# Kernel optimization log

Measured on AMD Instinct MI355X. Metric: run time of the kernel, lower is better.

The kernel has to match this reference:

```python
import jax, jax.numpy as jnp
import numpy as np

DIM = 256
HEADS = 8
WS = 8
N = WS * WS
HID = 1024
EPS = 1e-5


def _rel_pos_index():
    ch, cw = np.meshgrid(np.arange(WS), np.arange(WS), indexing='ij')
    coords = np.stack([ch.ravel(), cw.ravel()])  # [2, N]
    rel = coords[:, :, None] - coords[:, None, :]  # [2, N, N]
    rel = rel.transpose(1, 2, 0).astype(np.int64)
    rel[:, :, 0] += WS - 1
    rel[:, :, 1] += WS - 1
    rel[:, :, 0] *= 2 * WS - 1
    return jnp.asarray(rel.sum(-1))  # [N, N]

REL_IDX = _rel_pos_index()


def layer_norm(x, g, b):
    mu = jnp.mean(x, axis=-1, keepdims=True)
    var = jnp.mean(jnp.square(x - mu), axis=-1, keepdims=True)
    return (x - mu) * jax.lax.rsqrt(var + EPS) * g + b


def setup_inputs() -> dict:
    key = jax.random.key(0)
    ks = jax.random.split(key, 12)
    s = 0.02
    return {
        'x': jax.random.normal(ks[0], (32, 4096, DIM), jnp.float32),
        'attn_mask': jnp.zeros((64, N, N), jnp.float32),  # unused (forward sets mask=None)
        'g1': jnp.ones((DIM,), jnp.float32),
        'b1': jnp.zeros((DIM,), jnp.float32),
        'w_qkv': jax.random.normal(ks[1], (3 * DIM, DIM), jnp.float32) * s,
        'b_qkv': jnp.zeros((3 * DIM,), jnp.float32),
        'bias_table': jax.random.normal(ks[2], ((2 * WS - 1) ** 2, HEADS), jnp.float32) * s,
        'w_proj': jax.random.normal(ks[3], (DIM, DIM), jnp.float32) * s,
        'b_proj': jnp.zeros((DIM,), jnp.float32),
        'g2': jnp.ones((DIM,), jnp.float32),
        'b2': jnp.zeros((DIM,), jnp.float32),
        'w_fc1': jax.random.normal(ks[4], (HID, DIM), jnp.float32) * s,
        'b_fc1': jnp.zeros((HID,), jnp.float32),
        'w_fc2': jax.random.normal(ks[5], (DIM, HID), jnp.float32) * s,
        'b_fc2': jnp.zeros((DIM,), jnp.float32),
    }


def reference(x, attn_mask, g1, b1, w_qkv, b_qkv, bias_table, w_proj, b_proj,
              g2, b2, w_fc1, b_fc1, w_fc2, b_fc2):
    B, L, C = x.shape
    H = W = int(np.sqrt(L))
    hd = C // HEADS
    scale = hd ** -0.5

    shortcut = x
    xn = layer_norm(x, g1, b1).reshape(B, H, W, C)
    xw = xn.reshape(B, H // WS, WS, W // WS, WS, C)
    xw = xw.transpose(0, 1, 3, 2, 4, 5).reshape(-1, N, C)  # [B_, N, C]

    qkv = (xw @ w_qkv.T + b_qkv).reshape(-1, N, 3, HEADS, hd)
    q, k, v = [qkv[:, :, i].transpose(0, 2, 1, 3) for i in range(3)]  # [B_, h, N, d]
    attn = jnp.einsum('bhnd,bhmd->bhnm', q * scale, k)
    bias = bias_table[REL_IDX]  # [N, N, h]
    attn = attn + bias.transpose(2, 0, 1)[None]
    attn = jax.nn.softmax(attn, axis=-1)
    out = jnp.einsum('bhnm,bhmd->bhnd', attn, v)
    out = out.transpose(0, 2, 1, 3).reshape(-1, N, C)
    out = out @ w_proj.T + b_proj

    # window reverse
    out = out.reshape(B, H // WS, W // WS, WS, WS, C)
    out = out.transpose(0, 1, 3, 2, 4, 5).reshape(B, L, C)

    x1 = shortcut + out
    h = layer_norm(x1, g2, b2) @ w_fc1.T + b_fc1
    h = jax.nn.gelu(h, approximate=False)
    return x1 + (h @ w_fc2.T + b_fc2)
```

## Files before the change

kernel.cpp:

```cpp
#include <hip/hip_runtime.h>
#include <hip/hip_bf16.h>
#include <hip/hip_fp16.h>

typedef _Float16 f16;
typedef __attribute__((ext_vector_type(8))) _Float16 f16x8;
typedef __attribute__((ext_vector_type(4))) _Float16 f16x4;
typedef __attribute__((ext_vector_type(2))) _Float16 f16x2;
typedef __attribute__((ext_vector_type(4))) float f32x4;

#define AS1(p) ((const __attribute__((address_space(1))) void*)(p))
#define AS3(p) ((__attribute__((address_space(3))) void*)(p))

__global__ __launch_bounds__(256) void cvt_weights(
    const float* __restrict__ wq, const float* __restrict__ wp,
    const float* __restrict__ wf1, const float* __restrict__ wf2,
    f16* __restrict__ o) {
  int i = blockIdx.x * 256 + threadIdx.x;
  float v;
  if (i < 196608)       v = wq[i];
  else if (i < 262144)  v = wp[i - 196608];
  else if (i < 524288)  v = wf1[i - 262144];
  else                  v = wf2[i - 524288];
  o[i] = (f16)v;
}

__global__ __launch_bounds__(256) void prep_bias(
    const float* __restrict__ bt, float* __restrict__ T) {
  const int flat = blockIdx.x * 256 + threadIdx.x;
  const int h = flat >> 12, l = (flat >> 6) & 63, s = flat & 63;
  const int i = s >> 4, j = (s >> 2) & 3, r = s & 3;
  const int n = 16 * i + 4 * (l >> 4) + r;
  const int m = 16 * j + (l & 15);
  const int idx = ((n >> 3) - (m >> 3) + 7) * 15 + ((n & 7) - (m & 7) + 7);
  T[flat] = bt[idx * 8 + h] * 1.4426950408889634f;
}

template<bool PART, typename TIN>
__global__ __launch_bounds__(256) void ln_rows(
    const TIN* __restrict__ x, const float* __restrict__ g,
    const float* __restrict__ b, f16* __restrict__ out) {
  const int t = blockIdx.x * 4 + (threadIdx.x >> 6);
  const int lane = threadIdx.x & 63;
  float v0, v1, v2, v3;
  if constexpr (sizeof(TIN) == 4) {
    const float4 v = ((const float4*)(x + (long)t * 256))[lane];
    v0 = v.x; v1 = v.y; v2 = v.z; v3 = v.w;
  } else {
    const f16x4 v = ((const f16x4*)(x + (long)t * 256))[lane];
    v0 = (float)v[0]; v1 = (float)v[1]; v2 = (float)v[2]; v3 = (float)v[3];
  }
  float s  = v0 + v1 + v2 + v3;
  float ss = v0*v0 + v1*v1 + v2*v2 + v3*v3;
  #pragma unroll
  for (int off = 32; off; off >>= 1) {
    s  += __shfl_xor(s, off);
    ss += __shfl_xor(ss, off);
  }
  const float mu = s * (1.0f / 256.0f);
  const float var = ss * (1.0f / 256.0f) - mu * mu;
  const float rs = rsqrtf(var + 1e-5f);
  const float4 gv = ((const float4*)g)[lane];
  const float4 bv = ((const float4*)b)[lane];
  long row;
  if (PART) {
    const int bI = t >> 12, l = t & 4095;
    const int hh = l >> 6, w2 = l & 63;
    const int wi = bI * 64 + (hh >> 3) * 8 + (w2 >> 3);
    const int n  = (hh & 7) * 8 + (w2 & 7);
    row = (long)wi * 64 + n;
  } else {
    row = t;
  }
  f16x4 o4;
  o4[0] = (f16)((v0 - mu) * rs * gv.x + bv.x);
  o4[1] = (f16)((v1 - mu) * rs * gv.y + bv.y);
  o4[2] = (f16)((v2 - mu) * rs * gv.z + bv.z);
  o4[3] = (f16)((v3 - mu) * rs * gv.w + bv.w);
  *(f16x4*)(out + row * 256 + lane * 4) = o4;
}

template<int EPI, int K>
__global__ __launch_bounds__(256) void gemm_bt(
    const f16* __restrict__ A, const f16* __restrict__ Bw,
    const float* __restrict__ bias, const float* __restrict__ residf,
    const f16* __restrict__ residh,
    f16* __restrict__ outh, float* __restrict__ outf, int N) {
  __shared__ f16 As[2][128 * 64];
  __shared__ f16 Bs[2][128 * 64];
  const int tid  = threadIdx.x;
  const int wid  = tid >> 6;
  const int lane = tid & 63;
  const int qd   = lane >> 4;
  const int l16  = lane & 15;
  const int gx  = gridDim.x;
  const int nwg = gx * gridDim.y;
  const int g   = blockIdx.y * gx + blockIdx.x;
  const int gs  = (g & 7) * (nwg >> 3) + (g >> 3);
  const long tM = (long)(gs / gx) * 128;
  const int  tN = (gs % gx) * 128;
  const int sgrow = lane >> 3;
  const int scol  = ((lane & 7) ^ sgrow) * 8;
  const int wm = (wid >> 1) * 64;
  const int wn = (wid & 1) * 64;

  f32x4 acc[4][4];
  #pragma unroll
  for (int i = 0; i < 4; ++i)
    #pragma unroll
    for (int j = 0; j < 4; ++j) acc[i][j] = (f32x4){0.f, 0.f, 0.f, 0.f};

  const int nt = K / 64;
  f16x8 af[2][4], bf[2][4];

  auto stage_tile = [&](int tt) {
    const int k0 = tt * 64;
    f16* Ad = &As[tt & 1][0];
    f16* Bd = &Bs[tt & 1][0];
    #pragma unroll
    for (int u = 0; u < 4; ++u) {
      const int gidx = wid * 4 + u;
      const int row  = gidx * 8 + sgrow;
      __builtin_amdgcn_global_load_lds(AS1(A + (tM + row) * K + k0 + scol),
                                       AS3(&Ad[gidx * 512]), 16, 0, 0);
      __builtin_amdgcn_global_load_lds(AS1(Bw + (long)(tN + row) * K + k0 + scol),
                                       AS3(&Bd[gidx * 512]), 16, 0, 0);
    }
  };
  auto load_frags = [&](int cb) {
    #pragma unroll
    for (int kk = 0; kk < 2; ++kk) {
      #pragma unroll
      for (int i = 0; i < 4; ++i) {
        const int row = wm + i * 16 + l16;
        af[kk][i] = *(const f16x8*)&As[cb][row * 64 + (((kk << 2) | qd) ^ (row & 7)) * 8];
      }
      #pragma unroll
      for (int j = 0; j < 4; ++j) {
        const int row = wn + j * 16 + l16;
        bf[kk][j] = *(const f16x8*)&Bs[cb][row * 64 + (((kk << 2) | qd) ^ (row & 7)) * 8];
      }
    }
  };
  auto do_mfma = [&]() {
    #pragma unroll
    for (int kk = 0; kk < 2; ++kk)
      #pragma unroll
      for (int i = 0; i < 4; ++i)
        #pragma unroll
        for (int j = 0; j < 4; ++j)
          acc[i][j] = __builtin_amdgcn_mfma_f32_16x16x32_f16(af[kk][i], bf[kk][j], acc[i][j], 0, 0, 0);
  };

  stage_tile(0);
  stage_tile(1);

  for (int t = 0; t < nt - 2; ++t) {
    asm volatile("s_waitcnt vmcnt(8)" ::: "memory");
    __builtin_amdgcn_s_barrier();
    load_frags(t & 1);
    asm volatile("s_waitcnt lgkmcnt(0)" ::: "memory");
    __builtin_amdgcn_s_barrier();
    stage_tile(t + 2);
    do_mfma();
  }
  asm volatile("s_waitcnt vmcnt(8)" ::: "memory");
  __builtin_amdgcn_s_barrier();
  load_frags(nt & 1);
  do_mfma();
  asm volatile("s_waitcnt vmcnt(0)" ::: "memory");
  __builtin_amdgcn_s_barrier();
  load_frags((nt - 1) & 1);
  do_mfma();

  float bb[4];
  #pragma unroll
  for (int j = 0; j < 4; ++j) bb[j] = bias[tN + wn + j * 16 + l16];

  if (EPI == 3) {
    #pragma unroll
    for (int j = 0; j < 4; ++j) {
      const int col = tN + wn + j * 16 + l16;
      #pragma unroll
      for (int i = 0; i < 4; ++i) {
        #pragma unroll
        for (int r = 0; r < 4; ++r) {
          const long row = tM + wm + i * 16 + qd * 4 + r;
          const long off = row * 256 + col;
          outf[off] = (float)residh[off] + acc[i][j][r] + bb[j];
        }
      }
    }
  } else {
    __syncthreads();
    f16* slice = &As[0][0] + wid * 1024;
    const int rrow = lane >> 3;
    const int seg  = lane & 7;
    #pragma unroll
    for (int i = 0; i < 4; ++i) {
      #pragma unroll
      for (int j = 0; j < 4; ++j) {
        #pragma unroll
        for (int r = 0; r < 4; ++r) {
          float v = acc[i][j][r] + bb[j];
          if (EPI == 2) {
            const float u2 = v * v;
            const float w  = v * (-2.3022082f - 0.10294324f * u2);
            const float e  = __builtin_amdgcn_exp2f(w);
            v = v * __builtin_amdgcn_rcpf(1.0f + e);
          }
          const int r16 = qd * 4 + r;
          slice[r16 * 64 + ((j * 16 + l16) ^ ((r16 & 7) << 3))] = (f16)v;
        }
      }
      __syncthreads();
      #pragma unroll
      for (int hrow = 0; hrow < 16; hrow += 8) {
        const int lrow = hrow + rrow;
        const f16x8 v8 = *(const f16x8*)(slice + lrow * 64 + (seg ^ (lrow & 7)) * 8);
        const long grow = tM + wm + i * 16 + lrow;
        const int  gc   = tN + wn + seg * 8;
        if (EPI == 1) {
          const int rw = (int)grow;
          const int wi = rw >> 6, n = rw & 63;
          const int bI = wi >> 6, wloc = wi & 63;
          const int hh = (wloc >> 3) * 8 + (n >> 3);
          const int w2 = (wloc & 7) * 8 + (n & 7);
          const long prow = (long)bI * 4096 + hh * 64 + w2;
          const float* rp = residf + prow * 256 + gc;
          f16x8 o;
          #pragma unroll
          for (int k = 0; k < 8; ++k) o[k] = (f16)(rp[k] + (float)v8[k]);
          *(f16x8*)(outh + prow * 256 + gc) = o;
        } else {
          *(f16x8*)(outh + grow * N + gc) = v8;
        }
      }
      __syncthreads();
    }
  }
}

__global__ __launch_bounds__(256, 3) void attn_win(
    const f16* __restrict__ qkv, const float* __restrict__ bt,
    f16* __restrict__ out) {
  __shared__ __align__(16) char SMEM[4 * 12800];
  const int wid = threadIdx.x >> 6, lane = threadIdx.x & 63;
  const int qd = lane >> 4, l16 = lane & 15;
  const int unit = blockIdx.x * 4 + wid;
  const int wi = unit >> 3, h = unit & 7;
  char* W = SMEM + wid * 12800;
  f16* VT = (f16*)W;
  char* Pb = W + 4608;

  const f16* qbase = qkv + (long)wi * 64 * 768 + h * 32;

  f16x8 qa[4], kb[4];
  #pragma unroll
  for (int i = 0; i < 4; ++i)
    qa[i] = *(const f16x8*)(qbase + (16 * i + l16) * 768 + qd * 8);
  #pragma unroll
  for (int j = 0; j < 4; ++j)
    kb[j] = *(const f16x8*)(qbase + 256 + (16 * j + l16) * 768 + qd * 8);

  #pragma unroll
  for (int it = 0; it < 4; ++it) {
    const f16x8 v8 = *(const f16x8*)(qbase + 512 + (16 * it + l16) * 768 + qd * 8);
    #pragma unroll
    for (int e = 0; e < 8; ++e)
      VT[(qd * 8 + e) * 72 + 16 * it + l16] = v8[e];
  }

  f32x4 S[4][4];
  #pragma unroll
  for (int i = 0; i < 4; ++i)
    #pragma unroll
    for (int j = 0; j < 4; ++j) S[i][j] = (f32x4){0.f, 0.f, 0.f, 0.f};
  #pragma unroll
  for (int i = 0; i < 4; ++i)
    #pragma unroll
    for (int j = 0; j < 4; ++j)
      S[i][j] = __builtin_amdgcn_mfma_f32_16x16x32_f16(qa[i], kb[j], S[i][j], 0, 0, 0);

  const float SC = 0.17677669529663687f * 1.4426950408889634f;
  const float* Tb = bt + ((h * 64 + lane) << 6);
  #pragma unroll
  for (int i = 0; i < 4; ++i) {
    f32x4 b0 = *(const f32x4*)(Tb + i * 16);
    f32x4 b1 = *(const f32x4*)(Tb + i * 16 + 4);
    f32x4 b2 = *(const f32x4*)(Tb + i * 16 + 8);
    f32x4 b3 = *(const f32x4*)(Tb + i * 16 + 12);
    #pragma unroll
    for (int r = 0; r < 4; ++r) {
      S[i][0][r] = S[i][0][r] * SC + b0[r];
      S[i][1][r] = S[i][1][r] * SC + b1[r];
      S[i][2][r] = S[i][2][r] * SC + b2[r];
      S[i][3][r] = S[i][3][r] * SC + b3[r];
    }
  }

  float inv[4][4];
  #pragma unroll
  for (int i = 0; i < 4; ++i) {
    #pragma unroll
    for (int r = 0; r < 4; ++r) {
      float mx = fmaxf(fmaxf(S[i][0][r], S[i][1][r]), fmaxf(S[i][2][r], S[i][3][r]));
      #pragma unroll
      for (int msk = 1; msk < 16; msk <<= 1) mx = fmaxf(mx, __shfl_xor(mx, msk));
      float s0 = 0.f;
      #pragma unroll
      for (int j = 0; j < 4; ++j) {
        const float p = __builtin_amdgcn_exp2f(S[i][j][r] - mx);
        S[i][j][r] = p;
        s0 += p;
      }
      #pragma unroll
      for (int msk = 1; msk < 16; msk <<= 1) s0 += __shfl_xor(s0, msk);
      inv[i][r] = __builtin_amdgcn_rcpf(s0);
    }
  }

  #pragma unroll
  for (int i = 0; i < 4; ++i) {
    #pragma unroll
    for (int r = 0; r < 4; ++r) {
      const int n = 16 * i + 4 * qd + r;
      char* rowp = Pb + n * 128;
      const int sw = (n & 7) << 4;
      #pragma unroll
      for (int j = 0; j < 4; ++j)
        *(f16*)(rowp + ((j * 32 + l16 * 2) ^ sw)) = (f16)S[i][j][r];
    }
  }

  f32x4 O[4][2];
  #pragma unroll
  for (int i = 0; i < 4; ++i) {
    O[i][0] = (f32x4){0.f, 0.f, 0.f, 0.f};
    O[i][1] = (f32x4){0.f, 0.f, 0.f, 0.f};
  }
  #pragma unroll
  for (int kk = 0; kk < 2; ++kk) {
    f16x8 vb[2];
    #pragma unroll
    for (int jj = 0; jj < 2; ++jj)
      vb[jj] = *(const f16x8*)((const char*)W + (16 * jj + l16) * 144 + kk * 64 + qd * 16);
    #pragma unroll
    for (int i = 0; i < 4; ++i) {
      const f16x8 pa = *(const f16x8*)(Pb + (16 * i + l16) * 128 +
                                       ((kk * 64 + qd * 16) ^ ((l16 & 7) << 4)));
      #pragma unroll
      for (int jj = 0; jj < 2; ++jj)
        O[i][jj] = __builtin_amdgcn_mfma_f32_16x16x32_f16(pa, vb[jj], O[i][jj], 0, 0, 0);
    }
  }

  #pragma unroll
  for (int i = 0; i < 4; ++i) {
    #pragma unroll
    for (int jj = 0; jj < 2; ++jj) {
      #pragma unroll
      for (int r = 0; r < 4; ++r) {
        const int n = 16 * i + 4 * qd + r;
        *(f16*)(Pb + n * 80 + jj * 32 + l16 * 2) = (f16)(O[i][jj][r] * inv[i][r]);
      }
    }
  }
  #pragma unroll
  for (int it = 0; it < 4; ++it) {
    const int row = 16 * it + l16;
    const f16x8 o8 = *(const f16x8*)(Pb + row * 80 + qd * 16);
    *(f16x8*)(out + ((long)wi * 64 + row) * 256 + h * 32 + qd * 8) = o8;
  }
}

extern "C" void kernel_launch(void* const* d_in, const int* in_sizes, int n_in,
                              void* d_out, int out_size, void* d_ws, size_t ws_size,
                              hipStream_t stream) {
  const float* x     = (const float*)d_in[0];
  const float* g1    = (const float*)d_in[2];
  const float* b1    = (const float*)d_in[3];
  const float* wqkv  = (const float*)d_in[4];
  const float* bqkv  = (const float*)d_in[5];
  const float* btab  = (const float*)d_in[6];
  const float* wproj = (const float*)d_in[7];
  const float* bproj = (const float*)d_in[8];
  const float* g2    = (const float*)d_in[9];
  const float* b2    = (const float*)d_in[10];
  const float* wfc1  = (const float*)d_in[11];
  const float* bfc1  = (const float*)d_in[12];
  const float* wfc2  = (const float*)d_in[13];
  const float* bfc2  = (const float*)d_in[14];
  float* out = (float*)d_out;

  char* ws = (char*)d_ws;
  f16* wgt   = (f16*)ws;
  f16* wq16  = wgt;
  f16* wp16  = wgt + 196608;
  f16* wf116 = wgt + 262144;
  f16* wf216 = wgt + 524288;
  float* Tbuf = (float*)(ws + 1572864);

  int CH = 1;
  for (int cand = 32; cand >= 1; cand >>= 1) {
    const size_t need = 2097152ULL + (size_t)cand * 12582912ULL;
    if (need <= ws_size) { CH = cand; break; }
  }
  const int NC = 32 / CH;

  const size_t O_xn  = 2097152ULL;
  const size_t O_qkv = O_xn  + (size_t)CH * 2097152ULL;
  const size_t O_x1  = O_qkv + (size_t)CH * 6291456ULL;
  const size_t O_xn2 = O_x1  + (size_t)CH * 2097152ULL;
  f16* xnw  = (f16*)(ws + O_xn);
  f16* qkvb = (f16*)(ws + O_qkv);
  f16* x1h  = (f16*)(ws + O_x1);
  f16* xn2  = (f16*)(ws + O_xn2);
  f16* hbuf = (f16*)(ws + O_xn);

  cvt_weights<<<3072, 256, 0, stream>>>(wqkv, wproj, wfc1, wfc2, wgt);
  prep_bias<<<128, 256, 0, stream>>>(btab, Tbuf);

  const long imgElems = 4096L * 256;
  for (int c = 0; c < NC; ++c) {
    const float* xc  = x   + (long)c * CH * imgElems;
    float*       oc  = out + (long)c * CH * imgElems;
    ln_rows<true, float><<<CH * 1024, 256, 0, stream>>>(xc, g1, b1, xnw);
    gemm_bt<0, 256><<<dim3(6, CH * 32), 256, 0, stream>>>(xnw, wq16, bqkv, nullptr, nullptr, qkvb, nullptr, 768);
    attn_win<<<CH * 128, 256, 0, stream>>>(qkvb, Tbuf, xnw);
    gemm_bt<1, 256><<<dim3(2, CH * 32), 256, 0, stream>>>(xnw, wp16, bproj, xc, nullptr, x1h, nullptr, 256);
    ln_rows<false, f16><<<CH * 1024, 256, 0, stream>>>(x1h, g2, b2, xn2);
    gemm_bt<2, 256><<<dim3(8, CH * 32), 256, 0, stream>>>(xn2, wf116, bfc1, nullptr, nullptr, hbuf, nullptr, 1024);
    gemm_bt<3, 1024><<<dim3(2, CH * 32), 256, 0, stream>>>(hbuf, wf216, bfc2, nullptr, x1h, nullptr, oc, 256);
  }
}
```

Baseline: 775.1 us.

## Fuse FC1, GELU and FC2 into one kernel keeping hidden activations in LDS

Replaces the two MLP GEMM launches with a single fused kernel. Each 512-thread block loads a 128-row tile of normalized input into LDS, computes the hidden layer in 256-column chunks with GELU, stores each chunk to LDS, and accumulates FC2 directly. This removes the global write and read of the 4x-wide hidden tensor. In exchange, weight fragments are read straight from global memory without LDS staging or pipelining, the kernel uses 128KB of LDS, and the grid is only 32 blocks per image.

```diff
diff --git a/kernel.cpp b/kernel.cpp
--- a/kernel.cpp
+++ b/kernel.cpp
@@ -176,66 +176,158 @@
   #pragma unroll
   for (int j = 0; j < 4; ++j) bb[j] = bias[tN + wn + j * 16 + l16];
 
-  if (EPI == 3) {
+  __syncthreads();
+  f16* slice = &As[0][0] + wid * 1024;
+  const int rrow = lane >> 3;
+  const int seg  = lane & 7;
+  #pragma unroll
+  for (int i = 0; i < 4; ++i) {
     #pragma unroll
     for (int j = 0; j < 4; ++j) {
-      const int col = tN + wn + j * 16 + l16;
+      #pragma unroll
+      for (int r = 0; r < 4; ++r) {
+        float v = acc[i][j][r] + bb[j];
+        const int r16 = qd * 4 + r;
+        slice[r16 * 64 + ((j * 16 + l16) ^ ((r16 & 7) << 3))] = (f16)v;
+      }
+    }
+    __syncthreads();
+    #pragma unroll
+    for (int hrow = 0; hrow < 16; hrow += 8) {
+      const int lrow = hrow + rrow;
+      const f16x8 v8 = *(const f16x8*)(slice + lrow * 64 + (seg ^ (lrow & 7)) * 8);
+      const long grow = tM + wm + i * 16 + lrow;
+      const int  gc   = tN + wn + seg * 8;
+      if (EPI == 1) {
+        const int rw = (int)grow;
+        const int wi = rw >> 6, n = rw & 63;
+        const int bI = wi >> 6, wloc = wi & 63;
+        const int hh = (wloc >> 3) * 8 + (n >> 3);
+        const int w2 = (wloc & 7) * 8 + (n & 7);
+        const long prow = (long)bI * 4096 + hh * 64 + w2;
+        const float* rp = residf + prow * 256 + gc;
+        f16x8 o;
+        #pragma unroll
+        for (int k = 0; k < 8; ++k) o[k] = (f16)(rp[k] + (float)v8[k]);
+        *(f16x8*)(outh + prow * 256 + gc) = o;
+      } else {
+        *(f16x8*)(outh + grow * N + gc) = v8;
+      }
+    }
+    __syncthreads();
+  }
+}
+
+__global__ __launch_bounds__(512, 2) void ffn_fused(
+    const f16* __restrict__ A, const f16* __restrict__ w1, const f16* __restrict__ w2,
+    const float* __restrict__ b1f, const float* __restrict__ b2f,
+    const f16* __restrict__ residh, float* __restrict__ outf) {
+  __shared__ f16 As[128 * 256];
+  __shared__ f16 Hs[128 * 256];
+  const int tid = threadIdx.x;
+  const int wid = tid >> 6, lane = tid & 63;
+  const int qd = lane >> 4, l16 = lane & 15;
+  const int wm = (wid >> 2) * 64, wn = (wid & 3) * 64;
+  const int nwg = gridDim.x;
+  const int g = blockIdx.x;
+  const int gs = (g & 7) * (nwg >> 3) + (g >> 3);
+  const long tM = (long)gs * 128;
+
+  #pragma unroll
+  for (int u = 0; u < 8; ++u) {
+    const int row = u * 16 + (tid >> 5);
+    const int c = tid & 31;
+    const int cs = (c & ~7) | ((c & 7) ^ (row & 7));
+    __builtin_amdgcn_global_load_lds(AS1(A + (tM + row) * 256 + cs * 8),
+                                     AS3(&As[row * 256 + c * 8]), 16, 0, 0);
+  }
+  asm volatile("s_waitcnt vmcnt(0)" ::: "memory");
+  __builtin_amdgcn_s_barrier();
+
+  f32x4 acc2[4][4];
+  #pragma unroll
+  for (int i = 0; i < 4; ++i)
+    #pragma unroll
+    for (int j = 0; j < 4; ++j) acc2[i][j] = (f32x4){0.f, 0.f, 0.f, 0.f};
+
+  for (int hc = 0; hc < 4; ++hc) {
+    f32x4 acch[4][4];
+    #pragma unroll
+    for (int i = 0; i < 4; ++i)
+      #pragma unroll
+      for (int j = 0; j < 4; ++j) acch[i][j] = (f32x4){0.f, 0.f, 0.f, 0.f};
+    #pragma unroll
+    for (int kk = 0; kk < 8; ++kk) {
+      f16x8 a4[4], b4[4];
+      #pragma unroll
+      for (int i = 0; i < 4; ++i) {
+        const int row = wm + i * 16 + l16;
+        const int cg = kk * 4 + qd;
+        const int cs = (cg & ~7) | ((cg & 7) ^ (row & 7));
+        a4[i] = *(const f16x8*)&As[row * 256 + cs * 8];
+      }
+      #pragma unroll
+      for (int j = 0; j < 4; ++j)
+        b4[j] = *(const f16x8*)(w1 + (long)(hc * 256 + wn + j * 16 + l16) * 256 + kk * 32 + qd * 8);
+      #pragma unroll
+      for (int i = 0; i < 4; ++i)
+        #pragma unroll
+        for (int j = 0; j < 4; ++j)
+          acch[i][j] = __builtin_amdgcn_mfma_f32_16x16x32_f16(a4[i], b4[j], acch[i][j], 0, 0, 0);
+    }
+    __syncthreads();
+    #pragma unroll
+    for (int j = 0; j < 4; ++j) {
+      const float bb1 = b1f[hc * 256 + wn + j * 16 + l16];
       #pragma unroll
       for (int i = 0; i < 4; ++i) {
         #pragma unroll
         for (int r = 0; r < 4; ++r) {
-          const long row = tM + wm + i * 16 + qd * 4 + r;
-          const long off = row * 256 + col;
-          outf[off] = (float)residh[off] + acc[i][j][r] + bb[j];
+          float v = acch[i][j][r] + bb1;
+          const float u2 = v * v;
+          const float w  = v * (-2.3022082f - 0.10294324f * u2);
+          const float e  = __builtin_amdgcn_exp2f(w);
+          v = v * __builtin_amdgcn_rcpf(1.0f + e);
+          const int r16 = qd * 4 + r;
+          const int row = wm + i * 16 + r16;
+          Hs[row * 256 + wn + ((j * 16 + l16) ^ ((r16 & 7) << 3))] = (f16)v;
         }
       }
     }
-  } else {
     __syncthreads();
-    f16* slice = &As[0][0] + wid * 1024;
-    const int rrow = lane >> 3;
-    const int seg  = lane & 7;
+    #pragma unroll
+    for (int kk = 0; kk < 8; ++kk) {
+      f16x8 ah[4], bh[4];
+      #pragma unroll
+      for (int i = 0; i < 4; ++i) {
+        const int row = wm + i * 16 + l16;
+        const int cg = kk * 4 + qd;
+        const int cs = (cg & ~7) | ((cg & 7) ^ (row & 7));
+        ah[i] = *(const f16x8*)&Hs[row * 256 + cs * 8];
+      }
+      #pragma unroll
+      for (int j = 0; j < 4; ++j)
+        bh[j] = *(const f16x8*)(w2 + (long)(wn + j * 16 + l16) * 1024 + hc * 256 + kk * 32 + qd * 8);
+      #pragma unroll
+      for (int i = 0; i < 4; ++i)
+        #pragma unroll
+        for (int j = 0; j < 4; ++j)
+          acc2[i][j] = __builtin_amdgcn_mfma_f32_16x16x32_f16(ah[i], bh[j], acc2[i][j], 0, 0, 0);
+    }
+  }
+
+  #pragma unroll
+  for (int j = 0; j < 4; ++j) {
+    const int col = wn + j * 16 + l16;
+    const float bb2 = b2f[col];
     #pragma unroll
     for (int i = 0; i < 4; ++i) {
       #pragma unroll
-      for (int j = 0; j < 4; ++j) {
-        #pragma unroll
-        for (int r = 0; r < 4; ++r) {
-          float v = acc[i][j][r] + bb[j];
-          if (EPI == 2) {
-            const float u2 = v * v;
-            const float w  = v * (-2.3022082f - 0.10294324f * u2);
-            const float e  = __builtin_amdgcn_exp2f(w);
-            v = v * __builtin_amdgcn_rcpf(1.0f + e);
-          }
-          const int r16 = qd * 4 + r;
-          slice[r16 * 64 + ((j * 16 + l16) ^ ((r16 & 7) << 3))] = (f16)v;
-        }
-      }
-      __syncthreads();
-      #pragma unroll
-      for (int hrow = 0; hrow < 16; hrow += 8) {
-        const int lrow = hrow + rrow;
-        const f16x8 v8 = *(const f16x8*)(slice + lrow * 64 + (seg ^ (lrow & 7)) * 8);
-        const long grow = tM + wm + i * 16 + lrow;
-        const int  gc   = tN + wn + seg * 8;
-        if (EPI == 1) {
-          const int rw = (int)grow;
-          const int wi = rw >> 6, n = rw & 63;
-          const int bI = wi >> 6, wloc = wi & 63;
-          const int hh = (wloc >> 3) * 8 + (n >> 3);
-          const int w2 = (wloc & 7) * 8 + (n & 7);
-          const long prow = (long)bI * 4096 + hh * 64 + w2;
-          const float* rp = residf + prow * 256 + gc;
-          f16x8 o;
-          #pragma unroll
-          for (int k = 0; k < 8; ++k) o[k] = (f16)(rp[k] + (float)v8[k]);
-          *(f16x8*)(outh + prow * 256 + gc) = o;
-        } else {
-          *(f16x8*)(outh + grow * N + gc) = v8;
-        }
-      }
-      __syncthreads();
+      for (int r = 0; r < 4; ++r) {
+        const long row = tM + wm + i * 16 + qd * 4 + r;
+        const long off = row * 256 + col;
+        outf[off] = (float)residh[off] + acc2[i][j][r] + bb2;
+      }
     }
   }
 }
@@ -415,7 +507,6 @@
   f16* qkvb = (f16*)(ws + O_qkv);
   f16* x1h  = (f16*)(ws + O_x1);
   f16* xn2  = (f16*)(ws + O_xn2);
-  f16* hbuf = (f16*)(ws + O_xn);
 
   cvt_weights<<<3072, 256, 0, stream>>>(wqkv, wproj, wfc1, wfc2, wgt);
   prep_bias<<<128, 256, 0, stream>>>(btab, Tbuf);
@@ -429,7 +520,6 @@
     attn_win<<<CH * 128, 256, 0, stream>>>(qkvb, Tbuf, xnw);
     gemm_bt<1, 256><<<dim3(2, CH * 32), 256, 0, stream>>>(xnw, wp16, bproj, xc, nullptr, x1h, nullptr, 256);
     ln_rows<false, f16><<<CH * 1024, 256, 0, stream>>>(x1h, g2, b2, xn2);
-    gemm_bt<2, 256><<<dim3(8, CH * 32), 256, 0, stream>>>(xn2, wf116, bfc1, nullptr, nullptr, hbuf, nullptr, 1024);
-    gemm_bt<3, 1024><<<dim3(2, CH * 32), 256, 0, stream>>>(hbuf, wf216, bfc2, nullptr, x1h, nullptr, oc, 256);
-  }
-}
+    ffn_fused<<<CH * 32, 512, 0, stream>>>(xn2, wf116, wf216, bfc1, bfc2, x1h, oc);
+  }
+}
```

Result: slower. 832.2 us (+7.4%).
